# Optimization experiments

Measured on AMD Instinct MI355X. Metric: run time of the kernel, lower is better.

The kernel has to match this reference:

```python
import jax, jax.numpy as jnp
import numpy as np

N_QUBITS = 12
FAST_DEPTH = 4
FAST_DECAY = 0.9
LATENT = 512
BATCH = 2048


def _apply_ry(state, theta, wire):
    # state: (B, 2**n) real; RY is a real rotation. PennyLane default.qubit:
    # wire 0 is the most-significant bit of the state index.
    B = state.shape[0]
    s = state.reshape(B, 1 << wire, 2, -1)
    h = theta * 0.5
    c = jnp.cos(h)[:, None, None]
    sn = jnp.sin(h)[:, None, None]
    s0, s1 = s[:, :, 0], s[:, :, 1]
    out = jnp.stack([c * s0 - sn * s1, sn * s0 + c * s1], axis=2)
    return out.reshape(state.shape)


def _apply_cnot_adjacent(state, wire):
    # CNOT with control=wire, target=wire+1 (nearest-neighbor chain)
    B = state.shape[0]
    s = state.reshape(B, 1 << wire, 2, 2, -1)
    out = jnp.stack([s[:, :, 0], s[:, :, 1, ::-1]], axis=2)
    return out.reshape(state.shape)


def _fwp_circuit(x, fast, n_qubits, n_outputs):
    # x: (B, n_qubits) RY encoding angles; fast: (B, depth, n_qubits)
    B = x.shape[0]
    dim = 1 << n_qubits
    # Hadamard layer on |0...0> -> uniform positive real amplitudes.
    state = jnp.full((B, dim), 2.0 ** (-n_qubits / 2), dtype=x.dtype)
    for w in range(n_qubits):
        state = _apply_ry(state, x[:, w], w)
    for layer in range(fast.shape[1]):
        for w in range(n_qubits - 1):
            state = _apply_cnot_adjacent(state, w)
        for w in range(n_qubits):
            state = _apply_ry(state, fast[:, layer, w], w)
    probs = state * state  # real state -> |amp|^2
    outs = []
    for w in range(n_outputs):
        p = probs.reshape(B, 1 << w, 2, -1)
        outs.append(p[:, :, 0].sum(axis=(1, 2)) - p[:, :, 1].sum(axis=(1, 2)))
    return jnp.stack(outs, axis=1)  # (B, n_outputs) PauliZ expvals


def setup_inputs() -> dict:
    key = jax.random.key(0)
    ks = jax.random.split(key, 6)
    n, depth, latent = N_QUBITS, FAST_DEPTH, LATENT
    return {
        "x_t": jax.random.normal(ks[0], (BATCH, n), jnp.float32),
        "fast_prev": jax.random.normal(ks[1], (BATCH, depth, n), jnp.float32) * 0.1,
        "W_enc": jax.random.normal(ks[2], (latent, n), jnp.float32) / np.sqrt(n).astype(np.float32),
        "b_enc": jnp.zeros((latent,), jnp.float32),
        "W_upd": jax.random.normal(ks[3], (depth * n, latent), jnp.float32) / np.sqrt(latent).astype(np.float32),
        "b_upd": jnp.zeros((depth * n,), jnp.float32),
        "W_ro": jax.random.normal(ks[4], (1, n), jnp.float32) / np.sqrt(n).astype(np.float32),
        "b_ro": jnp.zeros((1,), jnp.float32),
    }


def reference(x_t, fast_prev, W_enc, b_enc, W_upd, b_upd, W_ro, b_ro):
    latent = jnp.tanh(x_t @ W_enc.T + b_enc)
    delta = (latent @ W_upd.T + b_upd).reshape(x_t.shape[0], FAST_DEPTH, N_QUBITS)
    fast_next = FAST_DECAY * fast_prev + delta
    q_out = _fwp_circuit(x_t, fast_next, N_QUBITS, N_QUBITS)  # n_outputs = n_qubits
    y_t = q_out @ W_ro.T + b_ro
    return (y_t, fast_next)
```

## Files before the change

### kernel.cpp

```cpp
#include <hip/hip_runtime.h>

static constexpr int NQ    = 12;
static constexpr int DEPTH = 4;
static constexpr int LAT   = 512;
static constexpr int FAST  = DEPTH * NQ;
static constexpr float DECAY = 0.9f;
static constexpr int PPF   = 132;

using v2f = __attribute__((ext_vector_type(2))) float;


__device__ __forceinline__ constexpr int G6(int x)  { return (x ^ (x >> 1)) & 63; }

template<int CTRL>
__device__ __forceinline__ float dppf(float x){
    return __int_as_float(__builtin_amdgcn_mov_dpp(__float_as_int(x), CTRL, 0xF, 0xF, false));
}
template<int B> __device__ __forceinline__ float lexch(float x);
template<> __device__ __forceinline__ float lexch<0>(float x){ return dppf<0xB1>(x); }
template<> __device__ __forceinline__ float lexch<1>(float x){ return dppf<0x4E>(x); }
template<> __device__ __forceinline__ float lexch<2>(float x){ return dppf<0x141>(dppf<0x1B>(x)); }
template<> __device__ __forceinline__ float lexch<3>(float x){ return dppf<0x128>(x); }
template<> __device__ __forceinline__ float lexch<4>(float x){
    return __int_as_float(__builtin_amdgcn_ds_swizzle(__float_as_int(x), 0x401F));
}
template<int B> __device__ __forceinline__ v2f lexch2(v2f v){
    return (v2f){ lexch<B>(v.x), lexch<B>(v.y) };
}

template<int B>
__device__ __forceinline__ void lanewire2(v2f (&u)[64], v2f cc, v2f ssv){
    #pragma unroll
    for (int k = 0; k < 64; k++){
        v2f p = lexch2<B>(u[k]);
        u[k] = cc * u[k] + ssv * p;
    }
}

template<int BIT>
__device__ __forceinline__ void regwire2(v2f (&u)[64], v2f cc, v2f ss){
    constexpr int M = 1 << BIT;
    #pragma unroll
    for (int r = 0; r < 64; r++){
        if (!(r & M)){
            v2f a = u[r], b = u[r ^ M];
            u[r]     = cc * a - ss * b;
            u[r ^ M] = ss * a + cc * b;
        }
    }
}

__global__ __launch_bounds__(64, 1)
void fwp_kernel(const float* __restrict__ x_t,
                const float* __restrict__ fast_prev,
                const float* __restrict__ W_enc,
                const float* __restrict__ b_enc,
                const float* __restrict__ W_upd,
                const float* __restrict__ b_upd,
                const float* __restrict__ W_ro,
                const float* __restrict__ b_ro,
                float* __restrict__ out_y,
                float* __restrict__ out_fast) {
    const int lane = threadIdx.x;
    const int eA   = 2 * blockIdx.x;
    const int eB   = eA + 1;

    __shared__ __align__(16) float Xs[64 * PPF];
    __shared__ __align__(8)  v2f CC[FAST], SS[FAST];

    float* latA = Xs;
    float* latB = Xs + LAT;

    float xaA[NQ], xaB[NQ];
    #pragma unroll
    for (int k = 0; k < NQ; k++) {
        xaA[k] = x_t[eA * NQ + k];
        xaB[k] = x_t[eB * NQ + k];
    }

    {
        const float4* we = (const float4*)(W_enc + lane * 8 * NQ);
        float4 be0 = *(const float4*)&b_enc[8 * lane];
        float4 be1 = *(const float4*)&b_enc[8 * lane + 4];
        float be[8] = {be0.x, be0.y, be0.z, be0.w, be1.x, be1.y, be1.z, be1.w};
        float lA[8], lB[8];
        #pragma unroll
        for (int t = 0; t < 8; t++) {
            float4 a0 = we[3 * t], a1 = we[3 * t + 1], a2 = we[3 * t + 2];
            float sA = be[t]
                + a0.x * xaA[0] + a0.y * xaA[1] + a0.z * xaA[2]  + a0.w * xaA[3]
                + a1.x * xaA[4] + a1.y * xaA[5] + a1.z * xaA[6]  + a1.w * xaA[7]
                + a2.x * xaA[8] + a2.y * xaA[9] + a2.z * xaA[10] + a2.w * xaA[11];
            float sB = be[t]
                + a0.x * xaB[0] + a0.y * xaB[1] + a0.z * xaB[2]  + a0.w * xaB[3]
                + a1.x * xaB[4] + a1.y * xaB[5] + a1.z * xaB[6]  + a1.w * xaB[7]
                + a2.x * xaB[8] + a2.y * xaB[9] + a2.z * xaB[10] + a2.w * xaB[11];
            lA[t] = tanhf(sA);
            lB[t] = tanhf(sB);
        }
        *(float4*)&latA[8 * lane]     = (float4){lA[0], lA[1], lA[2], lA[3]};
        *(float4*)&latA[8 * lane + 4] = (float4){lA[4], lA[5], lA[6], lA[7]};
        *(float4*)&latB[8 * lane]     = (float4){lB[0], lB[1], lB[2], lB[3]};
        *(float4*)&latB[8 * lane + 4] = (float4){lB[4], lB[5], lB[6], lB[7]};
    }

    if (lane < FAST) {
        const float4* wr = (const float4*)(W_upd + lane * LAT);
        const float4* la = (const float4*)(latA);
        const float4* lb = (const float4*)(latB);
        float base = b_upd[lane];
        float sA = base, sB = base;
        #pragma unroll 8
        for (int j = 0; j < LAT / 4; j++) {
            float4 w4 = wr[j];
            float4 a4 = la[j];
            float4 b4 = lb[j];
            sA += w4.x * a4.x + w4.y * a4.y + w4.z * a4.z + w4.w * a4.w;
            sB += w4.x * b4.x + w4.y * b4.y + w4.z * b4.z + w4.w * b4.w;
        }
        float angA = DECAY * fast_prev[eA * FAST + lane] + sA;
        float angB = DECAY * fast_prev[eB * FAST + lane] + sB;
        out_fast[eA * FAST + lane] = angA;
        out_fast[eB * FAST + lane] = angB;
        CC[lane] = (v2f){__cosf(0.5f * angA), __cosf(0.5f * angB)};
        SS[lane] = (v2f){__sinf(0.5f * angA), __sinf(0.5f * angB)};
    }

    v2f u[64];
    {
        v2f g0[NQ], g1[NQ];
        #pragma unroll
        for (int w = 0; w < NQ; w++) {
            float hA = 0.5f * xaA[w], hB = 0.5f * xaB[w];
            float cA = __cosf(hA), sA = __sinf(hA);
            float cB = __cosf(hB), sB = __sinf(hB);
            const float K = 0.70710678118654752f;
            g0[w] = (v2f){(cA - sA) * K, (cB - sB) * K};
            g1[w] = (v2f){(cA + sA) * K, (cB + sB) * K};
        }
        v2f L = (v2f){1.0f, 1.0f};
        #pragma unroll
        for (int w = 0; w < 6; w++)
            L *= ((lane >> (5 - w)) & 1) ? g1[w] : g0[w];
        u[0] = L;
        #pragma unroll
        for (int w = 6; w < NQ; w++) {
            const int S = 1 << (11 - w);
            #pragma unroll
            for (int r = 0; r < 64; r += 2 * S) {
                u[r + S] = u[r] * g1[w];
                u[r]     = u[r] * g0[w];
            }
        }
    }

    const int g    = G6(lane);
    const int gp   = g ^ 48;
    const int off2 = (lane & 1) * 64;
    const float* s_lo = Xs + g  * PPF + off2;
    const float* s_hi = Xs + g  * PPF + (off2 ^ 64);
    const float* p_lo = Xs + gp * PPF + off2;
    const float* p_hi = Xs + gp * PPF + (off2 ^ 64);
    float* wrow = Xs + lane * PPF;

    #pragma unroll 1
    for (int layer = 0; layer < DEPTH; layer++) {
        v2f cc[NQ], ss[NQ];
        #pragma unroll
        for (int w = 0; w < NQ; w++) { cc[w] = CC[layer * NQ + w]; ss[w] = SS[layer * NQ + w]; }
        v2f ss0 = (lane & 32) ? ss[0] : -ss[0];

        #pragma unroll
        for (int k = 0; k < 32; k++)
            *(float4*)&wrow[4 * k] =
                (float4){u[2 * k].x, u[2 * k].y, u[2 * k + 1].x, u[2 * k + 1].y};

        #pragma unroll
        for (int b = 0; b < 16; b++) {
            const int q = b ^ (b >> 1);
            const float* ps = (q < 8) ? s_lo + 8 * q : s_hi + 8 * (q - 8);
            const float* pq = (q < 8) ? p_lo + 8 * q : p_hi + 8 * (q - 8);
            float4 sa = *(const float4*)ps, sb = *(const float4*)(ps + 4);
            float4 pa = *(const float4*)pq, pb = *(const float4*)(pq + 4);
            v2f w0 = {sa.x, sa.y}, w1 = {sa.z, sa.w}, w2v = {sb.x, sb.y}, w3 = {sb.z, sb.w};
            v2f p0 = {pa.x, pa.y}, p1 = {pa.z, pa.w}, p2v = {pb.x, pb.y}, p3 = {pb.z, pb.w};
            if ((b & 1) == 0) {
                u[4 * b + 0] = cc[0] * w0  + ss0 * p0;
                u[4 * b + 1] = cc[0] * w1  + ss0 * p1;
                u[4 * b + 2] = cc[0] * w3  + ss0 * p3;
                u[4 * b + 3] = cc[0] * w2v + ss0 * p2v;
            } else {
                u[4 * b + 0] = cc[0] * w2v + ss0 * p2v;
                u[4 * b + 1] = cc[0] * w3  + ss0 * p3;
                u[4 * b + 2] = cc[0] * w1  + ss0 * p1;
                u[4 * b + 3] = cc[0] * w0  + ss0 * p0;
            }
        }

        { v2f sv = (lane & 16) ? ss[1] : -ss[1]; lanewire2<4>(u, cc[1], sv); }
        { v2f sv = (lane &  8) ? ss[2] : -ss[2]; lanewire2<3>(u, cc[2], sv); }
        { v2f sv = (lane &  4) ? ss[3] : -ss[3]; lanewire2<2>(u, cc[3], sv); }
        { v2f sv = (lane &  2) ? ss[4] : -ss[4]; lanewire2<1>(u, cc[4], sv); }
        { v2f sv = (lane &  1) ? ss[5] : -ss[5]; lanewire2<0>(u, cc[5], sv); }

        regwire2<5>(u, cc[6],  ss[6]);
        regwire2<4>(u, cc[7],  ss[7]);
        regwire2<3>(u, cc[8],  ss[8]);
        regwire2<2>(u, cc[9],  ss[9]);
        regwire2<1>(u, cc[10], ss[10]);
        regwire2<0>(u, cc[11], ss[11]);
    }

    float wro[NQ];
    #pragma unroll
    for (int w = 0; w < NQ; w++) wro[w] = W_ro[w];
    float sl = 0.0f;
    #pragma unroll
    for (int w = 0; w < 6; w++)
        sl += ((lane >> (5 - w)) & 1) ? -wro[w] : wro[w];

    v2f tot = (v2f){0.0f, 0.0f};
    v2f pw[6];
    #pragma unroll
    for (int k = 0; k < 6; k++) pw[k] = (v2f){0.0f, 0.0f};
    #pragma unroll
    for (int r = 0; r < 64; r++) {
        v2f p = u[r] * u[r];
        tot += p;
        pw[0] += (r & 32) ? -p : p;
        pw[1] += (r & 16) ? -p : p;
        pw[2] += (r & 8)  ? -p : p;
        pw[3] += (r & 4)  ? -p : p;
        pw[4] += (r & 2)  ? -p : p;
        pw[5] += (r & 1)  ? -p : p;
    }
    v2f y2 = (v2f){sl, sl} * tot;
    #pragma unroll
    for (int k = 0; k < 6; k++) y2 += (v2f){wro[6 + k], wro[6 + k]} * pw[k];
    float yA = y2.x, yB = y2.y;
    #pragma unroll
    for (int m = 32; m >= 1; m >>= 1) {
        yA += __shfl_xor(yA, m, 64);
        yB += __shfl_xor(yB, m, 64);
    }
    if (lane == 0) {
        float br = b_ro[0];
        out_y[eA] = yA + br;
        out_y[eB] = yB + br;
    }
}

extern "C" void kernel_launch(void* const* d_in, const int* in_sizes, int n_in,
                              void* d_out, int out_size, void* d_ws, size_t ws_size,
                              hipStream_t stream) {
    const float* x_t       = (const float*)d_in[0];
    const float* fast_prev = (const float*)d_in[1];
    const float* W_enc     = (const float*)d_in[2];
    const float* b_enc     = (const float*)d_in[3];
    const float* W_upd     = (const float*)d_in[4];
    const float* b_upd     = (const float*)d_in[5];
    const float* W_ro      = (const float*)d_in[6];
    const float* b_ro      = (const float*)d_in[7];
    float* out = (float*)d_out;

    fwp_kernel<<<1024, 64, 0, stream>>>(x_t, fast_prev, W_enc, b_enc,
                                        W_upd, b_upd, W_ro, b_ro,
                                        out , out + 2048 );
}
```

Baseline: 117.3 us.

## Swap qubit-to-lane/register mapping and replace LDS CNOT permutation with bpermute

Changes how qubits map to the state: the high wires now index registers and the low wires index lanes. The CNOT chain, formerly done as a write to shared memory and a permuted read back, is now a register-level cycle permutation combined with ds_bpermute lane gathers. Lane-wire rotations on bits 32 and 16 use v_permlane32/16_swap with an algebraic rewrite, and the rest use DPP. This drops the large LDS staging buffer and its write/read traffic. In exchange it adds 128 bpermute ops per layer, and the inline asm depends on gfx950-specific permlane swap instructions.

```diff
diff --git a/kernel.cpp b/kernel.cpp
--- a/kernel.cpp
+++ b/kernel.cpp
@@ -5,47 +5,41 @@
 static constexpr int LAT   = 512;
 static constexpr int FAST  = DEPTH * NQ;
 static constexpr float DECAY = 0.9f;
-static constexpr int PPF   = 132;
 
 using v2f = __attribute__((ext_vector_type(2))) float;
 
 
-__device__ __forceinline__ constexpr int G6(int x)  { return (x ^ (x >> 1)) & 63; }
-
+__device__ __forceinline__ constexpr int G6(int x){ return (x ^ (x >> 1)) & 63; }
+
+__device__ __forceinline__ float bperm(int idx, float v){
+    return __int_as_float(__builtin_amdgcn_ds_bpermute(idx, __float_as_int(v)));
+}
 template<int CTRL>
 __device__ __forceinline__ float dppf(float x){
     return __int_as_float(__builtin_amdgcn_mov_dpp(__float_as_int(x), CTRL, 0xF, 0xF, false));
 }
-template<int B> __device__ __forceinline__ float lexch(float x);
-template<> __device__ __forceinline__ float lexch<0>(float x){ return dppf<0xB1>(x); }
-template<> __device__ __forceinline__ float lexch<1>(float x){ return dppf<0x4E>(x); }
-template<> __device__ __forceinline__ float lexch<2>(float x){ return dppf<0x141>(dppf<0x1B>(x)); }
-template<> __device__ __forceinline__ float lexch<3>(float x){ return dppf<0x128>(x); }
-template<> __device__ __forceinline__ float lexch<4>(float x){
-    return __int_as_float(__builtin_amdgcn_ds_swizzle(__float_as_int(x), 0x401F));
-}
-template<int B> __device__ __forceinline__ v2f lexch2(v2f v){
-    return (v2f){ lexch<B>(v.x), lexch<B>(v.y) };
-}
-
-template<int B>
-__device__ __forceinline__ void lanewire2(v2f (&u)[64], v2f cc, v2f ssv){
-    #pragma unroll
-    for (int k = 0; k < 64; k++){
-        v2f p = lexch2<B>(u[k]);
-        u[k] = cc * u[k] + ssv * p;
-    }
-}
-
-template<int BIT>
-__device__ __forceinline__ void regwire2(v2f (&u)[64], v2f cc, v2f ss){
-    constexpr int M = 1 << BIT;
+template<int CTRL>
+__device__ __forceinline__ v2f dpp2(v2f v){ return (v2f){dppf<CTRL>(v.x), dppf<CTRL>(v.y)}; }
+
+__device__ __forceinline__ float xsum32(float x){
+    float a = x, b = x;
+    asm("v_permlane32_swap_b32 %0, %1" : "+v"(a), "+v"(b));
+    return a + b;
+}
+__device__ __forceinline__ float xsum16(float x){
+    float a = x, b = x;
+    asm("v_permlane16_swap_b32 %0, %1" : "+v"(a), "+v"(b));
+    return a + b;
+}
+
+template<int S>
+__device__ __forceinline__ void rw(v2f (&u)[64], v2f cc, v2f ss){
     #pragma unroll
     for (int r = 0; r < 64; r++){
-        if (!(r & M)){
-            v2f a = u[r], b = u[r ^ M];
+        if (!(r & S)){
+            v2f a = u[r], b = u[r | S];
             u[r]     = cc * a - ss * b;
-            u[r ^ M] = ss * a + cc * b;
+            u[r | S] = ss * a + cc * b;
         }
     }
 }
@@ -65,11 +59,8 @@
     const int eA   = 2 * blockIdx.x;
     const int eB   = eA + 1;
 
-    __shared__ __align__(16) float Xs[64 * PPF];
+    __shared__ __align__(16) float latA[LAT], latB[LAT];
     __shared__ __align__(8)  v2f CC[FAST], SS[FAST];
-
-    float* latA = Xs;
-    float* latB = Xs + LAT;
 
     float xaA[NQ], xaB[NQ];
     #pragma unroll
@@ -140,12 +131,12 @@
         }
         v2f L = (v2f){1.0f, 1.0f};
         #pragma unroll
-        for (int w = 0; w < 6; w++)
-            L *= ((lane >> (5 - w)) & 1) ? g1[w] : g0[w];
+        for (int w = 6; w < NQ; w++)
+            L *= ((lane >> (11 - w)) & 1) ? g1[w] : g0[w];
         u[0] = L;
         #pragma unroll
-        for (int w = 6; w < NQ; w++) {
-            const int S = 1 << (11 - w);
+        for (int w = 0; w < 6; w++) {
+            const int S = 32 >> w;
             #pragma unroll
             for (int r = 0; r < 64; r += 2 * S) {
                 u[r + S] = u[r] * g1[w];
@@ -154,70 +145,102 @@
         }
     }
 
-    const int g    = G6(lane);
-    const int gp   = g ^ 48;
-    const int off2 = (lane & 1) * 64;
-    const float* s_lo = Xs + g  * PPF + off2;
-    const float* s_hi = Xs + g  * PPF + (off2 ^ 64);
-    const float* p_lo = Xs + gp * PPF + off2;
-    const float* p_hi = Xs + gp * PPF + (off2 ^ 64);
-    float* wrow = Xs + lane * PPF;
+    const int idxA = G6(lane) * 4;
+    const int idxB = idxA ^ 128;
+
+    #define SIG1(h, src) { const int idx_ = ((h) & 1) ? idxB : idxA; \
+        u[h] = (v2f){ bperm(idx_, (src).x), bperm(idx_, (src).y) }; }
 
     #pragma unroll 1
     for (int layer = 0; layer < DEPTH; layer++) {
         v2f cc[NQ], ss[NQ];
         #pragma unroll
         for (int w = 0; w < NQ; w++) { cc[w] = CC[layer * NQ + w]; ss[w] = SS[layer * NQ + w]; }
-        v2f ss0 = (lane & 32) ? ss[0] : -ss[0];
-
-        #pragma unroll
-        for (int k = 0; k < 32; k++)
-            *(float4*)&wrow[4 * k] =
-                (float4){u[2 * k].x, u[2 * k].y, u[2 * k + 1].x, u[2 * k + 1].y};
-
-        #pragma unroll
-        for (int b = 0; b < 16; b++) {
-            const int q = b ^ (b >> 1);
-            const float* ps = (q < 8) ? s_lo + 8 * q : s_hi + 8 * (q - 8);
-            const float* pq = (q < 8) ? p_lo + 8 * q : p_hi + 8 * (q - 8);
-            float4 sa = *(const float4*)ps, sb = *(const float4*)(ps + 4);
-            float4 pa = *(const float4*)pq, pb = *(const float4*)(pq + 4);
-            v2f w0 = {sa.x, sa.y}, w1 = {sa.z, sa.w}, w2v = {sb.x, sb.y}, w3 = {sb.z, sb.w};
-            v2f p0 = {pa.x, pa.y}, p1 = {pa.z, pa.w}, p2v = {pb.x, pb.y}, p3 = {pb.z, pb.w};
-            if ((b & 1) == 0) {
-                u[4 * b + 0] = cc[0] * w0  + ss0 * p0;
-                u[4 * b + 1] = cc[0] * w1  + ss0 * p1;
-                u[4 * b + 2] = cc[0] * w3  + ss0 * p3;
-                u[4 * b + 3] = cc[0] * w2v + ss0 * p2v;
-            } else {
-                u[4 * b + 0] = cc[0] * w2v + ss0 * p2v;
-                u[4 * b + 1] = cc[0] * w3  + ss0 * p3;
-                u[4 * b + 2] = cc[0] * w1  + ss0 * p1;
-                u[4 * b + 3] = cc[0] * w0  + ss0 * p0;
-            }
-        }
-
-        { v2f sv = (lane & 16) ? ss[1] : -ss[1]; lanewire2<4>(u, cc[1], sv); }
-        { v2f sv = (lane &  8) ? ss[2] : -ss[2]; lanewire2<3>(u, cc[2], sv); }
-        { v2f sv = (lane &  4) ? ss[3] : -ss[3]; lanewire2<2>(u, cc[3], sv); }
-        { v2f sv = (lane &  2) ? ss[4] : -ss[4]; lanewire2<1>(u, cc[4], sv); }
-        { v2f sv = (lane &  1) ? ss[5] : -ss[5]; lanewire2<0>(u, cc[5], sv); }
-
-        regwire2<5>(u, cc[6],  ss[6]);
-        regwire2<4>(u, cc[7],  ss[7]);
-        regwire2<3>(u, cc[8],  ss[8]);
-        regwire2<2>(u, cc[9],  ss[9]);
-        regwire2<1>(u, cc[10], ss[10]);
-        regwire2<0>(u, cc[11], ss[11]);
-    }
+
+        SIG1(0, u[0]);  SIG1(1, u[1]);
+        { v2f t = u[2]; SIG1(2, u[3]); SIG1(3, t); }
+        { v2f t = u[4]; SIG1(4, u[6]);  SIG1(6, u[5]);  SIG1(5, u[7]);  SIG1(7, t); }
+        { v2f t = u[8]; SIG1(8, u[12]); SIG1(12, u[10]); SIG1(10, u[15]); SIG1(15, t); }
+        { v2f t = u[9]; SIG1(9, u[13]); SIG1(13, u[11]); SIG1(11, u[14]); SIG1(14, t); }
+        { v2f t = u[16]; SIG1(16, u[24]); SIG1(24, u[20]); SIG1(20, u[30]); SIG1(30, u[17]);
+                         SIG1(17, u[25]); SIG1(25, u[21]); SIG1(21, u[31]); SIG1(31, t); }
+        { v2f t = u[18]; SIG1(18, u[27]); SIG1(27, u[22]); SIG1(22, u[29]); SIG1(29, u[19]);
+                         SIG1(19, u[26]); SIG1(26, u[23]); SIG1(23, u[28]); SIG1(28, t); }
+        { v2f t = u[32]; SIG1(32, u[48]); SIG1(48, u[40]); SIG1(40, u[60]); SIG1(60, u[34]);
+                         SIG1(34, u[51]); SIG1(51, u[42]); SIG1(42, u[63]); SIG1(63, t); }
+        { v2f t = u[33]; SIG1(33, u[49]); SIG1(49, u[41]); SIG1(41, u[61]); SIG1(61, u[35]);
+                         SIG1(35, u[50]); SIG1(50, u[43]); SIG1(43, u[62]); SIG1(62, t); }
+        { v2f t = u[36]; SIG1(36, u[54]); SIG1(54, u[45]); SIG1(45, u[59]); SIG1(59, u[38]);
+                         SIG1(38, u[53]); SIG1(53, u[47]); SIG1(47, u[56]); SIG1(56, t); }
+        { v2f t = u[37]; SIG1(37, u[55]); SIG1(55, u[44]); SIG1(44, u[58]); SIG1(58, u[39]);
+                         SIG1(39, u[52]); SIG1(52, u[46]); SIG1(46, u[57]); SIG1(57, t); }
+
+        {
+            v2f sv = (lane & 32) ? ss[6] : -ss[6];
+            v2f cm = cc[6] - sv;
+            #pragma unroll
+            for (int h = 0; h < 64; h++) {
+                v2f s2 = (v2f){ xsum32(u[h].x), xsum32(u[h].y) };
+                u[h] = cm * u[h] + sv * s2;
+            }
+        }
+        {
+            v2f sv = (lane & 16) ? ss[7] : -ss[7];
+            v2f cm = cc[7] - sv;
+            #pragma unroll
+            for (int h = 0; h < 64; h++) {
+                v2f s2 = (v2f){ xsum16(u[h].x), xsum16(u[h].y) };
+                u[h] = cm * u[h] + sv * s2;
+            }
+        }
+        {
+            v2f sv = (lane & 8) ? ss[8] : -ss[8];
+            #pragma unroll
+            for (int h = 0; h < 64; h++) {
+                v2f p = dpp2<0x128>(u[h]);
+                u[h] = cc[8] * u[h] + sv * p;
+            }
+        }
+        {
+            v2f sv = (lane & 4) ? ss[9] : -ss[9];
+            #pragma unroll
+            for (int h = 0; h < 64; h++) {
+                v2f p = dpp2<0x141>(dpp2<0x1B>(u[h]));
+                u[h] = cc[9] * u[h] + sv * p;
+            }
+        }
+        {
+            v2f sv = (lane & 2) ? ss[10] : -ss[10];
+            #pragma unroll
+            for (int h = 0; h < 64; h++) {
+                v2f p = dpp2<0x4E>(u[h]);
+                u[h] = cc[10] * u[h] + sv * p;
+            }
+        }
+        {
+            v2f sv = (lane & 1) ? ss[11] : -ss[11];
+            #pragma unroll
+            for (int h = 0; h < 64; h++) {
+                v2f p = dpp2<0xB1>(u[h]);
+                u[h] = cc[11] * u[h] + sv * p;
+            }
+        }
+        rw<32>(u, cc[0], ss[0]);
+        rw<16>(u, cc[1], ss[1]);
+        rw<8> (u, cc[2], ss[2]);
+        rw<4> (u, cc[3], ss[3]);
+        rw<2> (u, cc[4], ss[4]);
+        rw<1> (u, cc[5], ss[5]);
+    }
+    #undef SIG1
 
     float wro[NQ];
     #pragma unroll
     for (int w = 0; w < NQ; w++) wro[w] = W_ro[w];
     float sl = 0.0f;
     #pragma unroll
-    for (int w = 0; w < 6; w++)
-        sl += ((lane >> (5 - w)) & 1) ? -wro[w] : wro[w];
+    for (int w = 6; w < NQ; w++)
+        sl += ((lane >> (11 - w)) & 1) ? -wro[w] : wro[w];
 
     v2f tot = (v2f){0.0f, 0.0f};
     v2f pw[6];
@@ -236,7 +259,7 @@
     }
     v2f y2 = (v2f){sl, sl} * tot;
     #pragma unroll
-    for (int k = 0; k < 6; k++) y2 += (v2f){wro[6 + k], wro[6 + k]} * pw[k];
+    for (int k = 0; k < 6; k++) y2 += (v2f){wro[k], wro[k]} * pw[k];
     float yA = y2.x, yB = y2.y;
     #pragma unroll
     for (int m = 32; m >= 1; m >>= 1) {
```

Result: faster. 114.3 us (-2.6%).
